# Kernel optimization log

Hardware: AMD Instinct MI355X
Metric: run time of the kernel (lower is better)

Reference implementation:

```python
import jax, jax.numpy as jnp
import numpy as np

S = 7          # grid size (7x7)
NUM_CLS = 20   # classes, channels 10:30


def _xyxy(box, m, n):
    # box: [B,4,H,W] with channels (x,y,w,h); faithful to source: x uses row idx m, y uses col idx n
    cx = (box[:, 0] + m) / S
    cy = (box[:, 1] + n) / S
    w, h = box[:, 2], box[:, 3]
    return cx - w / 2, cy - h / 2, cx + w / 2, cy + h / 2


def _iou(b1, b2):
    ix1 = jnp.maximum(b1[0], b2[0])
    iy1 = jnp.maximum(b1[1], b2[1])
    ix2 = jnp.minimum(b1[2], b2[2])
    iy2 = jnp.minimum(b1[3], b2[3])
    inter = jnp.clip(ix2 - ix1, 0.0) * jnp.clip(iy2 - iy1, 0.0)
    a1 = (b1[2] - b1[0]) * (b1[3] - b1[1])
    a2 = (b2[2] - b2[0]) * (b2[3] - b2[1])
    denom = a1 + a2 - inter
    pos = inter > 0
    return jnp.where(pos, inter / jnp.where(pos, denom, 1.0), 0.0)


def setup_inputs() -> dict:
    key = jax.random.key(0)
    k1, k2, k3 = jax.random.split(key, 3)
    B = 16384
    pred = jax.random.uniform(k1, (B, 30, S, S), dtype=jnp.float32) * 0.98 + 0.01
    lab = jax.random.uniform(k2, (B, 30, S, S), dtype=jnp.float32) * 0.9 + 0.05
    conf = (jax.random.uniform(k3, (B, S, S)) < 0.3).astype(jnp.float32)  # obj indicator, exactly 0/1
    lab = lab.at[:, 4].set(conf).at[:, 9].set(conf)
    lab = lab.at[:, 5:9].set(lab[:, 0:4])  # dataset duplicates the gt box for both predictors
    return {"pred": pred, "labels": lab}


def reference(pred, labels):
    B = labels.shape[0]
    m = jnp.arange(S, dtype=pred.dtype).reshape(S, 1)  # row index, broadcast over H axis
    n = jnp.arange(S, dtype=pred.dtype).reshape(1, S)  # col index, broadcast over W axis

    obj = (labels[:, 4] == 1).astype(pred.dtype)       # [B,H,W]
    noobj = 1.0 - obj

    b1 = _xyxy(pred[:, 0:4], m, n)
    b2 = _xyxy(pred[:, 5:9], m, n)
    gt = _xyxy(labels[:, 0:4], m, n)
    iou1 = _iou(b1, gt)
    iou2 = _iou(b2, gt)
    resp1 = (iou1 >= iou2).astype(pred.dtype)          # box1 responsible

    coor1 = 5.0 * (jnp.sum((pred[:, 0:2] - labels[:, 0:2]) ** 2, axis=1)
                   + jnp.sum((jnp.sqrt(pred[:, 2:4]) - jnp.sqrt(labels[:, 2:4])) ** 2, axis=1))
    coor2 = 5.0 * (jnp.sum((pred[:, 5:7] - labels[:, 5:7]) ** 2, axis=1)
                   + jnp.sum((jnp.sqrt(pred[:, 7:9]) - jnp.sqrt(labels[:, 7:9])) ** 2, axis=1))

    objc1 = (pred[:, 4] - iou1) ** 2
    objc2 = (pred[:, 9] - iou2) ** 2

    coor = resp1 * coor1 + (1 - resp1) * coor2
    obj_conf = resp1 * objc1 + (1 - resp1) * objc2
    noobj_resp = 0.5 * (resp1 * objc2 + (1 - resp1) * objc1)  # non-responsible box in obj cell
    cls = jnp.sum((pred[:, 10:] - labels[:, 10:]) ** 2, axis=1)

    noobj_cell = 0.5 * (pred[:, 4] ** 2 + pred[:, 9] ** 2)    # cells with no object

    loss = jnp.sum(obj * (coor + obj_conf + noobj_resp + cls)) + jnp.sum(noobj * noobj_cell)
    return loss / B
```

## Files before the change

kernel.cpp:

```cpp
#include <hip/hip_runtime.h>

#define S7 7
#define NCELL 49
#define CH 30
#define IMG_F (CH * NCELL)
#define K_IMG 2
#define BLK 512
#define NF4 (K_IMG * IMG_F / 4)
#define GRID 1024

typedef __attribute__((address_space(1))) const void global_cvoid;
typedef __attribute__((address_space(3))) void lds_void;

__global__ __launch_bounds__(BLK) void yolo_loss_stage1(
    const float4* __restrict__ pred4,
    const float4* __restrict__ lab4,
    float* __restrict__ partials,
    int npairs)
{
    __shared__ float4 sp4[NF4];
    __shared__ float4 sl4[NF4];
    const float* sp = (const float*)sp4;
    const float* sl = (const float*)sl4;

    const int tid = threadIdx.x;
    float contrib = 0.0f;

    for (int pair = blockIdx.x; pair < npairs; pair += gridDim.x) {
        const size_t g4base = (size_t)pair * NF4;
        for (int i = tid; i < NF4; i += BLK) {
            __builtin_amdgcn_global_load_lds(
                (global_cvoid*)(pred4 + g4base + i),
                (lds_void*)(&sp4[i]), 16, 0, 0);
            __builtin_amdgcn_global_load_lds(
                (global_cvoid*)(lab4 + g4base + i),
                (lds_void*)(&sl4[i]), 16, 0, 0);
        }
        __syncthreads();

        if (tid < K_IMG * NCELL) {
            const int img  = tid / NCELL;
            const int cell = tid - img * NCELL;
            const float* __restrict__ pb = sp + img * IMG_F + cell;
            const float* __restrict__ lb = sl + img * IMG_F + cell;

            float p[10], l[10];
            #pragma unroll
            for (int c = 0; c < 10; ++c) {
                p[c] = pb[c * NCELL];
                l[c] = lb[c * NCELL];
            }
            float cls = 0.0f;
            #pragma unroll
            for (int c = 10; c < CH; ++c) {
                float d = pb[c * NCELL] - lb[c * NCELL];
                cls += d * d;
            }

            const int   row = cell / S7;
            const float mi = (float)row;
            const float nj = (float)(cell - row * S7);
            const float invS = 1.0f / 7.0f;

            float ax1, ay1, ax2, ay2;
            {
                float cx = (p[0] + mi) * invS, cy = (p[1] + nj) * invS;
                ax1 = cx - 0.5f * p[2]; ay1 = cy - 0.5f * p[3];
                ax2 = cx + 0.5f * p[2]; ay2 = cy + 0.5f * p[3];
            }
            float bx1, by1, bx2, by2;
            {
                float cx = (p[5] + mi) * invS, cy = (p[6] + nj) * invS;
                bx1 = cx - 0.5f * p[7]; by1 = cy - 0.5f * p[8];
                bx2 = cx + 0.5f * p[7]; by2 = cy + 0.5f * p[8];
            }
            float gx1, gy1, gx2, gy2;
            {
                float cx = (l[0] + mi) * invS, cy = (l[1] + nj) * invS;
                gx1 = cx - 0.5f * l[2]; gy1 = cy - 0.5f * l[3];
                gx2 = cx + 0.5f * l[2]; gy2 = cy + 0.5f * l[3];
            }

            float iou1, iou2;
            {
                float ix1 = fmaxf(ax1, gx1), iy1 = fmaxf(ay1, gy1);
                float ix2 = fminf(ax2, gx2), iy2 = fminf(ay2, gy2);
                float inter = fmaxf(ix2 - ix1, 0.0f) * fmaxf(iy2 - iy1, 0.0f);
                float a1 = (ax2 - ax1) * (ay2 - ay1);
                float a2 = (gx2 - gx1) * (gy2 - gy1);
                float denom = a1 + a2 - inter;
                iou1 = (inter > 0.0f) ? inter / denom : 0.0f;
            }
            {
                float ix1 = fmaxf(bx1, gx1), iy1 = fmaxf(by1, gy1);
                float ix2 = fminf(bx2, gx2), iy2 = fminf(by2, gy2);
                float inter = fmaxf(ix2 - ix1, 0.0f) * fmaxf(iy2 - iy1, 0.0f);
                float a1 = (bx2 - bx1) * (by2 - by1);
                float a2 = (gx2 - gx1) * (gy2 - gy1);
                float denom = a1 + a2 - inter;
                iou2 = (inter > 0.0f) ? inter / denom : 0.0f;
            }

            const bool resp1 = (iou1 >= iou2);

            float d0 = p[0] - l[0], d1 = p[1] - l[1];
            float s2 = __builtin_sqrtf(p[2]) - __builtin_sqrtf(l[2]);
            float s3 = __builtin_sqrtf(p[3]) - __builtin_sqrtf(l[3]);
            float coor1 = 5.0f * (d0 * d0 + d1 * d1 + s2 * s2 + s3 * s3);

            float e0 = p[5] - l[5], e1 = p[6] - l[6];
            float t2 = __builtin_sqrtf(p[7]) - __builtin_sqrtf(l[7]);
            float t3 = __builtin_sqrtf(p[8]) - __builtin_sqrtf(l[8]);
            float coor2 = 5.0f * (e0 * e0 + e1 * e1 + t2 * t2 + t3 * t3);

            float o1 = p[4] - iou1; o1 *= o1;
            float o2 = p[9] - iou2; o2 *= o2;

            float coor       = resp1 ? coor1 : coor2;
            float obj_conf   = resp1 ? o1 : o2;
            float noobj_resp = 0.5f * (resp1 ? o2 : o1);
            float noobj_cell = 0.5f * (p[4] * p[4] + p[9] * p[9]);

            const bool obj = (l[4] == 1.0f);
            contrib += obj ? (coor + obj_conf + noobj_resp + cls) : noobj_cell;
        }
        __syncthreads();
    }

    #pragma unroll
    for (int off = 32; off > 0; off >>= 1)
        contrib += __shfl_down(contrib, off, 64);

    __shared__ float wsum[BLK / 64];
    const int lane = tid & 63;
    const int wid  = tid >> 6;
    if (lane == 0) wsum[wid] = contrib;
    __syncthreads();
    if (tid == 0) {
        float bs = 0.0f;
        #pragma unroll
        for (int w = 0; w < BLK / 64; ++w) bs += wsum[w];
        partials[blockIdx.x] = bs;
    }
}

__global__ __launch_bounds__(1024) void yolo_loss_stage2(
    const float* __restrict__ partials,
    float* __restrict__ out,
    int nparts, float inv_B)
{
    float s = (threadIdx.x < nparts) ? partials[threadIdx.x] : 0.0f;

    #pragma unroll
    for (int off = 32; off > 0; off >>= 1)
        s += __shfl_down(s, off, 64);

    __shared__ float wsum[16];
    const int lane = threadIdx.x & 63;
    const int wid  = threadIdx.x >> 6;
    if (lane == 0) wsum[wid] = s;
    __syncthreads();
    if (threadIdx.x == 0) {
        float bs = 0.0f;
        #pragma unroll
        for (int w = 0; w < 16; ++w) bs += wsum[w];
        out[0] = bs * inv_B;
    }
}

extern "C" void kernel_launch(void* const* d_in, const int* in_sizes, int n_in,
                              void* d_out, int out_size, void* d_ws, size_t ws_size,
                              hipStream_t stream) {
    const float4* pred4 = (const float4*)d_in[0];
    const float4* lab4  = (const float4*)d_in[1];
    float* out = (float*)d_out;
    float* partials = (float*)d_ws;

    const int B = in_sizes[0] / IMG_F;
    const int npairs = B / K_IMG;
    const int grid = (npairs < GRID) ? npairs : GRID;

    yolo_loss_stage1<<<grid, BLK, 0, stream>>>(pred4, lab4, partials, npairs);
    yolo_loss_stage2<<<1, 1024, 0, stream>>>(partials, out, grid, 1.0f / (float)B);
}
```

Before: 37.29 us.

## Double-buffer LDS tiles to overlap next pair's load with compute

Splits the shared-memory staging into two buffers and issues the async global-to-LDS loads for the next image pair before computing on the current one. Explicit vmcnt waits, sized per wave by how many loads it has in flight, replace the full syncthreads. The grid is also reduced so each block handles more tiles and gets more overlap. The cost is double the LDS per block, which may reduce occupancy, and hand-tuned waitcnt values that depend on the per-thread load count staying exactly as it is now.

```diff
diff --git a/kernel.cpp b/kernel.cpp
--- a/kernel.cpp
+++ b/kernel.cpp
@@ -7,7 +7,7 @@
 #define K_IMG 2
 #define BLK 512
 #define NF4 (K_IMG * IMG_F / 4)
-#define GRID 1024
+#define GRID 768
 
 typedef __attribute__((address_space(1))) const void global_cvoid;
 typedef __attribute__((address_space(3))) void lds_void;
@@ -18,27 +18,50 @@
     float* __restrict__ partials,
     int npairs)
 {
-    __shared__ float4 sp4[NF4];
-    __shared__ float4 sl4[NF4];
-    const float* sp = (const float*)sp4;
-    const float* sl = (const float*)sl4;
+    __shared__ float4 sp4[2][NF4];
+    __shared__ float4 sl4[2][NF4];
 
     const int tid = threadIdx.x;
+    const int wid = tid >> 6;
     float contrib = 0.0f;
 
-    for (int pair = blockIdx.x; pair < npairs; pair += gridDim.x) {
-        const size_t g4base = (size_t)pair * NF4;
-        for (int i = tid; i < NF4; i += BLK) {
-            __builtin_amdgcn_global_load_lds(
-                (global_cvoid*)(pred4 + g4base + i),
-                (lds_void*)(&sp4[i]), 16, 0, 0);
-            __builtin_amdgcn_global_load_lds(
-                (global_cvoid*)(lab4 + g4base + i),
-                (lds_void*)(&sl4[i]), 16, 0, 0);
+    #define STAGE(buf, pair)                                                     \
+        do {                                                                     \
+            const size_t g4_ = (size_t)(pair) * NF4;                             \
+            for (int i_ = tid; i_ < NF4; i_ += BLK) {                            \
+                __builtin_amdgcn_global_load_lds(                                \
+                    (global_cvoid*)(pred4 + g4_ + i_),                           \
+                    (lds_void*)(&sp4[buf][i_]), 16, 0, 0);                       \
+                __builtin_amdgcn_global_load_lds(                                \
+                    (global_cvoid*)(lab4 + g4_ + i_),                            \
+                    (lds_void*)(&sl4[buf][i_]), 16, 0, 0);                       \
+            }                                                                    \
+        } while (0)
+
+    const int bid = (int)blockIdx.x;
+    const int ntiles = (npairs - bid + GRID - 1) / GRID;
+
+    STAGE(0, bid);
+
+    for (int t = 0; t < ntiles; ++t) {
+        const int cur = t & 1;
+        const bool hasnext = (t + 1) < ntiles;
+
+        if (hasnext)
+            STAGE(cur ^ 1, bid + (t + 1) * GRID);
+
+        if (hasnext) {
+            if (wid < 4) asm volatile("s_waitcnt vmcnt(4)" ::: "memory");
+            else         asm volatile("s_waitcnt vmcnt(2)" ::: "memory");
+        } else {
+            asm volatile("s_waitcnt vmcnt(0)" ::: "memory");
         }
-        __syncthreads();
+        __builtin_amdgcn_sched_barrier(0);
+        __builtin_amdgcn_s_barrier();
 
         if (tid < K_IMG * NCELL) {
+            const float* __restrict__ sp = (const float*)sp4[cur];
+            const float* __restrict__ sl = (const float*)sl4[cur];
             const int img  = tid / NCELL;
             const int cell = tid - img * NCELL;
             const float* __restrict__ pb = sp + img * IMG_F + cell;
@@ -124,8 +147,10 @@
             const bool obj = (l[4] == 1.0f);
             contrib += obj ? (coor + obj_conf + noobj_resp + cls) : noobj_cell;
         }
-        __syncthreads();
+
+        __builtin_amdgcn_s_barrier();
     }
+    #undef STAGE
 
     #pragma unroll
     for (int off = 32; off > 0; off >>= 1)
@@ -133,7 +158,6 @@
 
     __shared__ float wsum[BLK / 64];
     const int lane = tid & 63;
-    const int wid  = tid >> 6;
     if (lane == 0) wsum[wid] = contrib;
     __syncthreads();
     if (tid == 0) {
```

New measurement: 37.77 us. No clear change (+1.3%).
